# Kernel optimization log

Hardware: AMD Instinct MI355X
Metric: run time of the kernel (lower is better)

Reference implementation:

```python
import jax, jax.numpy as jnp
import numpy as np

T, N, ENC_DIM, DEC_DIM, ATTN_DIM = 2048, 64, 1024, 1024, 256


def setup_inputs() -> dict:
    key = jax.random.key(0)
    k1, k2, k3, k4, k5 = jax.random.split(key, 5)
    enc_out = jax.random.normal(k1, (T, N, ENC_DIM), dtype=jnp.float32)
    dec_h = jax.random.normal(k2, (N, DEC_DIM), dtype=jnp.float32)
    # Linear weights stored as [out, in] like torch; scaled like default init
    W_e = jax.random.normal(k3, (ATTN_DIM, ENC_DIM), dtype=jnp.float32) / np.sqrt(ENC_DIM)
    W_d = jax.random.normal(k4, (ATTN_DIM, DEC_DIM), dtype=jnp.float32) / np.sqrt(DEC_DIM)
    v = jax.random.normal(k5, (1, ATTN_DIM), dtype=jnp.float32) / np.sqrt(ATTN_DIM)
    return {"enc_out": enc_out, "dec_h": dec_h, "W_e": W_e, "W_d": W_d, "v": v}


def reference(enc_out, dec_h, W_e, W_d, v):
    # e_proj: [T, N, A]; d_proj: [1, N, A]
    e_proj = jnp.einsum('tne,ae->tna', enc_out, W_e)
    d_proj = jnp.einsum('nd,ad->na', dec_h, W_d)[None, :, :]
    # scores: [T, N] = tanh(e+d) @ v
    scores = jnp.einsum('tna,a->tn', jnp.tanh(e_proj + d_proj), v[0])
    alpha = jax.nn.softmax(scores, axis=0)  # softmax over time dim
    ctx = jnp.einsum('tn,tne->ne', alpha, enc_out)  # [N, E]
    return (ctx, alpha)
```

## Files before the change

kernel.cpp:

```cpp
#include <hip/hip_runtime.h>
#include <math.h>

#define T_DIM 2048
#define N_DIM 64
#define E_DIM 1024
#define A_DIM 256
#define TCHUNK 32
#define NCHUNK (T_DIM / TCHUNK)

typedef __bf16 bf16x8 __attribute__((ext_vector_type(8)));
typedef __bf16 bf16x4 __attribute__((ext_vector_type(4)));
typedef float f32x4 __attribute__((ext_vector_type(4)));

__device__ __forceinline__ float tanh_fast(float x) {
    float xc = fminf(fmaxf(x, -15.f), 15.f);
    float e = __expf(2.f * xc);
    return (e - 1.f) / (e + 1.f);
}

__global__ __launch_bounds__(256) void convert_W(const float* __restrict__ W_e,
                                                 __bf16* __restrict__ Wp) {
    const int uid = blockIdx.x * 256 + threadIdx.x;
    const int a = uid >> 7;
    const int c = uid & 127;
    const float4* src = (const float4*)(W_e + (size_t)a * E_DIM + c * 8);
    float4 x0 = src[0], x1 = src[1];
    bf16x8 o;
    o[0] = (__bf16)x0.x; o[1] = (__bf16)x0.y; o[2] = (__bf16)x0.z; o[3] = (__bf16)x0.w;
    o[4] = (__bf16)x1.x; o[5] = (__bf16)x1.y; o[6] = (__bf16)x1.z; o[7] = (__bf16)x1.w;
    *(bf16x8*)(Wp + ((size_t)c * 256 + a) * 8) = o;
}

__global__ __launch_bounds__(256) void dproj_kernel(
    const float* __restrict__ dec_h, const float* __restrict__ W_d,
    float* __restrict__ d_proj) {
    __shared__ float dec[E_DIM];
    const int n = blockIdx.x;
    const int tid = threadIdx.x;
    reinterpret_cast<float4*>(dec)[tid] =
        reinterpret_cast<const float4*>(dec_h + (size_t)n * E_DIM)[tid];
    __syncthreads();
    const float* w = W_d + (size_t)tid * E_DIM;
    float acc = 0.f;
#pragma unroll 4
    for (int e = 0; e < E_DIM; e += 4) {
        float4 wv = *reinterpret_cast<const float4*>(w + e);
        acc = fmaf(wv.x, dec[e], acc);
        acc = fmaf(wv.y, dec[e + 1], acc);
        acc = fmaf(wv.z, dec[e + 2], acc);
        acc = fmaf(wv.w, dec[e + 3], acc);
    }
    d_proj[n * A_DIM + tid] = acc;
}

__global__ __launch_bounds__(512, 4) void flash_kernel(
    const float* __restrict__ enc, const __bf16* __restrict__ Wp,
    const float* __restrict__ dproj, const float* __restrict__ v,
    float* __restrict__ scores, float* __restrict__ partial,
    float* __restrict__ ms, float* __restrict__ zs) {
    __shared__ __align__(16) __bf16 Atile[TCHUNK * E_DIM];
    float* red = ((float*)Atile) + 16384 - 288;
    float* wls = red + 256;

    const int tid = threadIdx.x;
    const int bid = blockIdx.x;
    const int n = bid & (N_DIM - 1);
    const int c = bid >> 6;
    const int t0 = c * TCHUNK;
    const int wn = tid >> 6;
    const int lane = tid & 63;
    const int lr = lane & 15, lg = lane >> 4;

    f32x4 acc[2][2];
#pragma unroll
    for (int i = 0; i < 2; ++i)
#pragma unroll
        for (int j = 0; j < 2; ++j) acc[i][j] = (f32x4){0.f, 0.f, 0.f, 0.f};

    float vv[2], dp[2];
#pragma unroll
    for (int fn = 0; fn < 2; ++fn) {
        const int a = wn * 32 + fn * 16 + lr;
        vv[fn] = v[a];
        dp[fn] = dproj[n * A_DIM + a];
    }

    const int srow = tid >> 4, sg = tid & 15;
    const int sgg = (sg & 7) >> 1, sbh = sg & 1;
    const int sks = sg >> 3;
    const float* encRow =
        enc + ((size_t)(t0 + srow) * N_DIM + n) * E_DIM + sg * 4;
    const bf16x8* WpV = (const bf16x8*)Wp;

    float4 c0a = *(const float4*)encRow;
    float4 c0b = *(const float4*)(encRow + 64);

#pragma unroll 1
    for (int it = 0; it < 8; ++it) {
        {
            const int ks1 = it * 4 + sks, ks2 = ks1 + 2;
            bf16x4 w0, w1;
            w0[0] = (__bf16)c0a.x; w0[1] = (__bf16)c0a.y;
            w0[2] = (__bf16)c0a.z; w0[3] = (__bf16)c0a.w;
            w1[0] = (__bf16)c0b.x; w1[1] = (__bf16)c0b.y;
            w1[2] = (__bf16)c0b.z; w1[3] = (__bf16)c0b.w;
            const int u1 = ks1 * 128 + sgg * 32 + (srow ^ ((ks1 * 4 + sgg) & 7));
            const int u2 = ks2 * 128 + sgg * 32 + (srow ^ ((ks2 * 4 + sgg) & 7));
            *(bf16x4*)((char*)Atile + u1 * 16 + sbh * 8) = w0;
            *(bf16x4*)((char*)Atile + u2 * 16 + sbh * 8) = w1;
        }
        bf16x8 bfr[4][2];
#pragma unroll
        for (int s = 0; s < 4; ++s)
#pragma unroll
            for (int fn = 0; fn < 2; ++fn)
                bfr[s][fn] = WpV[(size_t)(it * 4 + s) * 1024 + lg * 256 +
                                 wn * 32 + fn * 16 + lr];
        float4 na, nb;
        if (it < 7) {
            const float* p = encRow + (it + 1) * 128;
            na = *(const float4*)p;
            nb = *(const float4*)(p + 64);
        }
        __syncthreads();
#pragma unroll
        for (int s = 0; s < 4; ++s) {
            const int ks = it * 4 + s;
#pragma unroll
            for (int fm = 0; fm < 2; ++fm) {
                const int u =
                    ks * 128 + lg * 32 + ((fm * 16 + lr) ^ ((ks * 4 + lg) & 7));
                bf16x8 af = *(const bf16x8*)((const char*)Atile + u * 16);
                acc[fm][0] = __builtin_amdgcn_mfma_f32_16x16x32_bf16(
                    af, bfr[s][0], acc[fm][0], 0, 0, 0);
                acc[fm][1] = __builtin_amdgcn_mfma_f32_16x16x32_bf16(
                    af, bfr[s][1], acc[fm][1], 0, 0, 0);
            }
        }
        c0a = na;
        c0b = nb;
    }

    float pr[2][4];
#pragma unroll
    for (int fm = 0; fm < 2; ++fm) {
#pragma unroll
        for (int reg = 0; reg < 4; ++reg) {
            float p = fmaf(vv[0], tanh_fast(acc[fm][0][reg] + dp[0]), 0.f);
            p = fmaf(vv[1], tanh_fast(acc[fm][1][reg] + dp[1]), p);
            p += __shfl_xor(p, 1);
            p += __shfl_xor(p, 2);
            p += __shfl_xor(p, 4);
            p += __shfl_xor(p, 8);
            pr[fm][reg] = p;
        }
    }
    __syncthreads();
    if (lr == 0) {
#pragma unroll
        for (int fm = 0; fm < 2; ++fm)
#pragma unroll
            for (int reg = 0; reg < 4; ++reg)
                red[wn * 32 + fm * 16 + lg * 4 + reg] = pr[fm][reg];
    }
    __syncthreads();
    if (tid < TCHUNK) {
        float s = 0.f;
#pragma unroll
        for (int w = 0; w < 8; ++w) s += red[w * 32 + tid];
        scores[(t0 + tid) * N_DIM + n] = s;
        if (partial) {
            float m = s;
            m = fmaxf(m, __shfl_xor(m, 1));
            m = fmaxf(m, __shfl_xor(m, 2));
            m = fmaxf(m, __shfl_xor(m, 4));
            m = fmaxf(m, __shfl_xor(m, 8));
            m = fmaxf(m, __shfl_xor(m, 16));
            float w = __expf(s - m);
            float Z = w;
            Z += __shfl_xor(Z, 1);
            Z += __shfl_xor(Z, 2);
            Z += __shfl_xor(Z, 4);
            Z += __shfl_xor(Z, 8);
            Z += __shfl_xor(Z, 16);
            wls[tid] = w;
            if (tid == 0) {
                ms[n * NCHUNK + c] = m;
                zs[n * NCHUNK + c] = Z;
            }
        }
    }
    __syncthreads();

    if (!partial) return;
    const int cs = tid >> 1, rh = tid & 1;
    const int ks = cs >> 3, gg = (cs >> 1) & 3, bh = cs & 1;
    const int colbase = ks * 32 + gg * 8 + bh * 4;
    f32x4 a4 = (f32x4){0.f, 0.f, 0.f, 0.f};
    if (cs < 250) {
        const int q = (ks * 4 + gg) & 7;
        const int ubase = ks * 128 + gg * 32;
#pragma unroll 4
        for (int r = rh * 16; r < rh * 16 + 16; ++r) {
            const float w = wls[r];
            bf16x4 ev = *(const bf16x4*)((const char*)Atile +
                                         (ubase + (r ^ q)) * 16 + bh * 8);
            a4[0] = fmaf(w, (float)ev[0], a4[0]);
            a4[1] = fmaf(w, (float)ev[1], a4[1]);
            a4[2] = fmaf(w, (float)ev[2], a4[2]);
            a4[3] = fmaf(w, (float)ev[3], a4[3]);
        }
    } else {
#pragma unroll 4
        for (int r = rh * 16; r < rh * 16 + 16; ++r) {
            const float w = wls[r];
            float4 ev = *(const float4*)(
                enc + ((size_t)(t0 + r) * N_DIM + n) * E_DIM + colbase);
            a4[0] = fmaf(w, ev.x, a4[0]);
            a4[1] = fmaf(w, ev.y, a4[1]);
            a4[2] = fmaf(w, ev.z, a4[2]);
            a4[3] = fmaf(w, ev.w, a4[3]);
        }
    }
#pragma unroll
    for (int k = 0; k < 4; ++k) a4[k] += __shfl_xor(a4[k], 1);
    if (rh == 0)
        *(f32x4*)(partial + ((size_t)c * N_DIM + n) * E_DIM + colbase) = a4;
}

__global__ __launch_bounds__(256) void combine_kernel(
    const float* __restrict__ partial, const float* __restrict__ ms,
    const float* __restrict__ zs, const float* __restrict__ scores,
    float* __restrict__ ctx, float* __restrict__ alpha) {
    __shared__ float scale[NCHUNK];
    __shared__ float MZ[2];
    const int n = blockIdx.x;
    const int tid = threadIdx.x;
    if (tid < NCHUNK) {
        float m = ms[n * NCHUNK + tid];
        float M = m;
        M = fmaxf(M, __shfl_xor(M, 1));
        M = fmaxf(M, __shfl_xor(M, 2));
        M = fmaxf(M, __shfl_xor(M, 4));
        M = fmaxf(M, __shfl_xor(M, 8));
        M = fmaxf(M, __shfl_xor(M, 16));
        M = fmaxf(M, __shfl_xor(M, 32));
        float e = __expf(m - M);
        float z = zs[n * NCHUNK + tid] * e;
        float Z = z;
        Z += __shfl_xor(Z, 1);
        Z += __shfl_xor(Z, 2);
        Z += __shfl_xor(Z, 4);
        Z += __shfl_xor(Z, 8);
        Z += __shfl_xor(Z, 16);
        Z += __shfl_xor(Z, 32);
        scale[tid] = e;
        if (tid == 0) {
            MZ[0] = M;
            MZ[1] = Z;
        }
    }
    __syncthreads();
    const float M = MZ[0];
    const float invZ = 1.f / MZ[1];
    f32x4 a4 = (f32x4){0.f, 0.f, 0.f, 0.f};
#pragma unroll 4
    for (int c = 0; c < NCHUNK; ++c) {
        const float s = scale[c] * invZ;
        float4 p = *(const float4*)(partial +
                                    ((size_t)c * N_DIM + n) * E_DIM + tid * 4);
        a4[0] = fmaf(s, p.x, a4[0]);
        a4[1] = fmaf(s, p.y, a4[1]);
        a4[2] = fmaf(s, p.z, a4[2]);
        a4[3] = fmaf(s, p.w, a4[3]);
    }
    *(f32x4*)(ctx + (size_t)n * E_DIM + tid * 4) = a4;
    for (int t = tid; t < T_DIM; t += 256)
        alpha[t * N_DIM + n] = __expf(scores[t * N_DIM + n] - M) * invZ;
}

__global__ __launch_bounds__(256) void softmax_kernel(
    const float* __restrict__ scores, float* __restrict__ alpha) {
    __shared__ float red[256];
    const int n = blockIdx.x;
    const int tid = threadIdx.x;
    float m = -3.4e38f;
    for (int t = tid; t < T_DIM; t += 256)
        m = fmaxf(m, scores[t * N_DIM + n]);
    red[tid] = m;
    __syncthreads();
    for (int s = 128; s; s >>= 1) {
        if (tid < s) red[tid] = fmaxf(red[tid], red[tid + s]);
        __syncthreads();
    }
    m = red[0];
    __syncthreads();
    float sum = 0.f;
    for (int t = tid; t < T_DIM; t += 256)
        sum += expf(scores[t * N_DIM + n] - m);
    red[tid] = sum;
    __syncthreads();
    for (int s = 128; s; s >>= 1) {
        if (tid < s) red[tid] += red[tid + s];
        __syncthreads();
    }
    const float inv = 1.f / red[0];
    for (int t = tid; t < T_DIM; t += 256)
        alpha[t * N_DIM + n] = expf(scores[t * N_DIM + n] - m) * inv;
}

__global__ __launch_bounds__(256) void ctx_f32(const float* __restrict__ enc,
                                               const float* __restrict__ alpha,
                                               float* __restrict__ ctx) {
    const int n = blockIdx.x;
    const int tid = threadIdx.x;
    float4 acc = {0.f, 0.f, 0.f, 0.f};
    for (int t = 0; t < T_DIM; ++t) {
        const float al = alpha[t * N_DIM + n];
        float4 ev = *reinterpret_cast<const float4*>(
            enc + (size_t)(t * N_DIM + n) * E_DIM + tid * 4);
        acc.x = fmaf(al, ev.x, acc.x);
        acc.y = fmaf(al, ev.y, acc.y);
        acc.z = fmaf(al, ev.z, acc.z);
        acc.w = fmaf(al, ev.w, acc.w);
    }
    *reinterpret_cast<float4*>(ctx + (size_t)n * E_DIM + tid * 4) = acc;
}

extern "C" void kernel_launch(void* const* d_in, const int* in_sizes, int n_in,
                              void* d_out, int out_size, void* d_ws,
                              size_t ws_size, hipStream_t stream) {
    const float* enc = (const float*)d_in[0];
    const float* dec_h = (const float*)d_in[1];
    const float* W_e = (const float*)d_in[2];
    const float* W_d = (const float*)d_in[3];
    const float* v = (const float*)d_in[4];

    float* out = (float*)d_out;
    float* ctx = out;
    float* alpha = out + 65536;

    float* ws = (float*)d_ws;
    float* d_proj = ws;
    float* scores = ws + 16384;
    __bf16* Wp = (__bf16*)(ws + 147456);
    float* ms = ws + 278528;
    float* zs = ws + 282624;
    float* partial = ws + 286720;

    const size_t need =
        (size_t)(286720 + NCHUNK * N_DIM * E_DIM) * sizeof(float);
    const bool big = ws_size >= need;

    convert_W<<<128, 256, 0, stream>>>(W_e, Wp);
    dproj_kernel<<<N_DIM, 256, 0, stream>>>(dec_h, W_d, d_proj);
    flash_kernel<<<T_DIM / TCHUNK * N_DIM, 512, 0, stream>>>(
        enc, Wp, d_proj, v, scores, big ? partial : nullptr, ms, zs);
    if (big) {
        combine_kernel<<<N_DIM, 256, 0, stream>>>(partial, ms, zs, scores,
                                                  ctx, alpha);
    } else {
        softmax_kernel<<<N_DIM, 256, 0, stream>>>(scores, alpha);
        ctx_f32<<<N_DIM, 256, 0, stream>>>(enc, alpha, ctx);
    }
}
```

Baseline: 232.9 us.

## Deepen enc prefetch to two stages, merge prep kernels, use lightweight LDS barrier

Merges the W_e bf16 conversion and the decoder projection into a single prep kernel, which removes one launch. In the flash kernel, the enc rows are now prefetched two iterations ahead instead of one, and the k-loop is fully unrolled, so global-load latency is better hidden behind the MFMA work. The __syncthreads is replaced by an inline s_waitcnt lgkmcnt(0) + s_barrier, which skips waiting on outstanding global loads. The cost is higher register pressure under launch_bounds(512,4), and the custom barrier depends on the compiler not reordering memory operations around it.

```diff
diff --git a/kernel.cpp b/kernel.cpp
--- a/kernel.cpp
+++ b/kernel.cpp
@@ -18,39 +18,43 @@
     return (e - 1.f) / (e + 1.f);
 }
 
-__global__ __launch_bounds__(256) void convert_W(const float* __restrict__ W_e,
-                                                 __bf16* __restrict__ Wp) {
-    const int uid = blockIdx.x * 256 + threadIdx.x;
-    const int a = uid >> 7;
-    const int c = uid & 127;
-    const float4* src = (const float4*)(W_e + (size_t)a * E_DIM + c * 8);
-    float4 x0 = src[0], x1 = src[1];
-    bf16x8 o;
-    o[0] = (__bf16)x0.x; o[1] = (__bf16)x0.y; o[2] = (__bf16)x0.z; o[3] = (__bf16)x0.w;
-    o[4] = (__bf16)x1.x; o[5] = (__bf16)x1.y; o[6] = (__bf16)x1.z; o[7] = (__bf16)x1.w;
-    *(bf16x8*)(Wp + ((size_t)c * 256 + a) * 8) = o;
-}
-
-__global__ __launch_bounds__(256) void dproj_kernel(
-    const float* __restrict__ dec_h, const float* __restrict__ W_d,
+__device__ __forceinline__ void lds_barrier() {
+    asm volatile("s_waitcnt lgkmcnt(0)\n\ts_barrier" ::: "memory");
+}
+
+__global__ __launch_bounds__(256) void prep_kernel(
+    const float* __restrict__ W_e, const float* __restrict__ dec_h,
+    const float* __restrict__ W_d, __bf16* __restrict__ Wp,
     float* __restrict__ d_proj) {
     __shared__ float dec[E_DIM];
-    const int n = blockIdx.x;
-    const int tid = threadIdx.x;
-    reinterpret_cast<float4*>(dec)[tid] =
-        reinterpret_cast<const float4*>(dec_h + (size_t)n * E_DIM)[tid];
-    __syncthreads();
-    const float* w = W_d + (size_t)tid * E_DIM;
-    float acc = 0.f;
+    const int tid = threadIdx.x;
+    if (blockIdx.x < 128) {
+        const int uid = blockIdx.x * 256 + tid;
+        const int a = uid >> 7;
+        const int c = uid & 127;
+        const float4* src = (const float4*)(W_e + (size_t)a * E_DIM + c * 8);
+        float4 x0 = src[0], x1 = src[1];
+        bf16x8 o;
+        o[0] = (__bf16)x0.x; o[1] = (__bf16)x0.y; o[2] = (__bf16)x0.z; o[3] = (__bf16)x0.w;
+        o[4] = (__bf16)x1.x; o[5] = (__bf16)x1.y; o[6] = (__bf16)x1.z; o[7] = (__bf16)x1.w;
+        *(bf16x8*)(Wp + ((size_t)c * 256 + a) * 8) = o;
+    } else {
+        const int n = blockIdx.x - 128;
+        reinterpret_cast<float4*>(dec)[tid] =
+            reinterpret_cast<const float4*>(dec_h + (size_t)n * E_DIM)[tid];
+        __syncthreads();
+        const float* w = W_d + (size_t)tid * E_DIM;
+        float acc = 0.f;
 #pragma unroll 4
-    for (int e = 0; e < E_DIM; e += 4) {
-        float4 wv = *reinterpret_cast<const float4*>(w + e);
-        acc = fmaf(wv.x, dec[e], acc);
-        acc = fmaf(wv.y, dec[e + 1], acc);
-        acc = fmaf(wv.z, dec[e + 2], acc);
-        acc = fmaf(wv.w, dec[e + 3], acc);
-    }
-    d_proj[n * A_DIM + tid] = acc;
+        for (int e = 0; e < E_DIM; e += 4) {
+            float4 wv = *reinterpret_cast<const float4*>(w + e);
+            acc = fmaf(wv.x, dec[e], acc);
+            acc = fmaf(wv.y, dec[e + 1], acc);
+            acc = fmaf(wv.z, dec[e + 2], acc);
+            acc = fmaf(wv.w, dec[e + 3], acc);
+        }
+        d_proj[n * A_DIM + tid] = acc;
+    }
 }
 
 __global__ __launch_bounds__(512, 4) void flash_kernel(
@@ -92,37 +96,39 @@
         enc + ((size_t)(t0 + srow) * N_DIM + n) * E_DIM + sg * 4;
     const bf16x8* WpV = (const bf16x8*)Wp;
 
-    float4 c0a = *(const float4*)encRow;
-    float4 c0b = *(const float4*)(encRow + 64);
-
-#pragma unroll 1
+    float4 pa = *(const float4*)encRow;
+    float4 pb = *(const float4*)(encRow + 64);
+    float4 qa = *(const float4*)(encRow + 128);
+    float4 qb = *(const float4*)(encRow + 192);
+
+#pragma unroll
     for (int it = 0; it < 8; ++it) {
+        bf16x8 bfr[4][2];
+#pragma unroll
+        for (int s = 0; s < 4; ++s)
+#pragma unroll
+            for (int fn = 0; fn < 2; ++fn)
+                bfr[s][fn] = WpV[(size_t)(it * 4 + s) * 1024 + lg * 256 +
+                                 wn * 32 + fn * 16 + lr];
         {
             const int ks1 = it * 4 + sks, ks2 = ks1 + 2;
             bf16x4 w0, w1;
-            w0[0] = (__bf16)c0a.x; w0[1] = (__bf16)c0a.y;
-            w0[2] = (__bf16)c0a.z; w0[3] = (__bf16)c0a.w;
-            w1[0] = (__bf16)c0b.x; w1[1] = (__bf16)c0b.y;
-            w1[2] = (__bf16)c0b.z; w1[3] = (__bf16)c0b.w;
+            w0[0] = (__bf16)pa.x; w0[1] = (__bf16)pa.y;
+            w0[2] = (__bf16)pa.z; w0[3] = (__bf16)pa.w;
+            w1[0] = (__bf16)pb.x; w1[1] = (__bf16)pb.y;
+            w1[2] = (__bf16)pb.z; w1[3] = (__bf16)pb.w;
             const int u1 = ks1 * 128 + sgg * 32 + (srow ^ ((ks1 * 4 + sgg) & 7));
             const int u2 = ks2 * 128 + sgg * 32 + (srow ^ ((ks2 * 4 + sgg) & 7));
             *(bf16x4*)((char*)Atile + u1 * 16 + sbh * 8) = w0;
             *(bf16x4*)((char*)Atile + u2 * 16 + sbh * 8) = w1;
         }
-        bf16x8 bfr[4][2];
-#pragma unroll
-        for (int s = 0; s < 4; ++s)
-#pragma unroll
-            for (int fn = 0; fn < 2; ++fn)
-                bfr[s][fn] = WpV[(size_t)(it * 4 + s) * 1024 + lg * 256 +
-                                 wn * 32 + fn * 16 + lr];
-        float4 na, nb;
-        if (it < 7) {
-            const float* p = encRow + (it + 1) * 128;
-            na = *(const float4*)p;
-            nb = *(const float4*)(p + 64);
-        }
-        __syncthreads();
+        float4 ra, rb;
+        if (it < 6) {
+            const float* p = encRow + (it + 2) * 128;
+            ra = *(const float4*)p;
+            rb = *(const float4*)(p + 64);
+        }
+        lds_barrier();
 #pragma unroll
         for (int s = 0; s < 4; ++s) {
             const int ks = it * 4 + s;
@@ -137,8 +143,8 @@
                     af, bfr[s][1], acc[fm][1], 0, 0, 0);
             }
         }
-        c0a = na;
-        c0b = nb;
+        pa = qa; pb = qb;
+        qa = ra; qb = rb;
     }
 
     float pr[2][4];
@@ -352,8 +358,7 @@
         (size_t)(286720 + NCHUNK * N_DIM * E_DIM) * sizeof(float);
     const bool big = ws_size >= need;
 
-    convert_W<<<128, 256, 0, stream>>>(W_e, Wp);
-    dproj_kernel<<<N_DIM, 256, 0, stream>>>(dec_h, W_d, d_proj);
+    prep_kernel<<<192, 256, 0, stream>>>(W_e, dec_h, W_d, Wp, d_proj);
     flash_kernel<<<T_DIM / TCHUNK * N_DIM, 512, 0, stream>>>(
         enc, Wp, d_proj, v, scores, big ? partial : nullptr, ms, zs);
     if (big) {
```

New measurement: 228.4 us. Within noise of the previous version (-1.9%).
